# Optimization experiments

Hardware: AMD Instinct MI355X
Metric: run time of the kernel (lower is better)

The kernel has to match this reference:

```python
import jax, jax.numpy as jnp
import numpy as np

B, T, DK, DV = 64, 2048, 128, 128
INIT_SCALE = 0.01


def setup_inputs() -> dict:
    key = jax.random.key(0)
    ks = jax.random.split(key, 7)
    return {
        "query": jax.random.normal(ks[0], (B, T, DK), dtype=jnp.float32),
        "key": jax.random.normal(ks[1], (B, T, DK), dtype=jnp.float32),
        "value": jax.random.normal(ks[2], (B, T, DV), dtype=jnp.float32),
        "alpha": jax.random.uniform(ks[3], (B, T, 1), dtype=jnp.float32),
        "rho": jax.random.uniform(ks[4], (B, T, 1), dtype=jnp.float32),
        "lam": jax.random.uniform(ks[5], (B, T, 1), dtype=jnp.float32),
        "init_state": jax.random.normal(ks[6], (B, DK, DV), dtype=jnp.float32) * INIT_SCALE,
    }


def reference(query, key, value, alpha, rho, lam, init_state):
    """Decayed outer-product fast-weight memory, scanned over time.

    Per step t:  M_t = lam_t * M_{t-1} + (rho_t * alpha_t) * (k_t outer v_t)
                 r_t = q_t^T M_t                      # [B, D_v]
    Returns readouts [B, T, D_v].
    """
    # time-major inputs for scan: [T, B, ...]
    tm = lambda x: jnp.swapaxes(x, 0, 1)
    xs = (tm(query), tm(key), tm(value), tm(alpha), tm(rho), tm(lam))

    def step(M, inp):
        q, k, v, a, r, l = inp  # q,k: [B,DK]; v: [B,DV]; a,r,l: [B,1]
        write_scale = (r * a)[:, :, None]          # [B,1,1]
        outer = k[:, :, None] * v[:, None, :]      # [B,DK,DV]
        M = l[:, :, None] * M + write_scale * outer
        read = jnp.einsum('bk,bkv->bv', q, M)      # [B,DV]
        return M, read

    _, reads = jax.lax.scan(step, init_state, xs)
    return jnp.swapaxes(reads, 0, 1)  # [B,T,DV]
```

## Files before the change

### kernel.cpp

```cpp
#include <hip/hip_runtime.h>
#include <hip/hip_bf16.h>


typedef float  f32x4  __attribute__((ext_vector_type(4)));
typedef short  bf16x8 __attribute__((ext_vector_type(8)));
typedef short  bf16x4 __attribute__((ext_vector_type(4)));

constexpr int B_ = 64, T_ = 2048;
constexpr int NSPLIT = 8;
constexpr int CT = 64;
constexpr int NCH = T_ / CT;

__device__ __forceinline__ bf16x8 cvt8(float4 a, float4 b) {
  union { __hip_bfloat162 h2[4]; bf16x8 v; } u;
  u.h2[0] = __float22bfloat162_rn(make_float2(a.x, a.y));
  u.h2[1] = __float22bfloat162_rn(make_float2(a.z, a.w));
  u.h2[2] = __float22bfloat162_rn(make_float2(b.x, b.y));
  u.h2[3] = __float22bfloat162_rn(make_float2(b.z, b.w));
  return u.v;
}

__device__ __forceinline__ float fexp2(float x) { return __builtin_exp2f(x); }
__device__ __forceinline__ float flog2(float x) { return __builtin_log2f(x); }

#define MFMA(a, b, c) __builtin_amdgcn_mfma_f32_16x16x32_bf16((a), (b), (c), 0, 0, 0)

__global__ __launch_bounds__(256, 2) void lmm_2b(
    const float* __restrict__ q_g, const float* __restrict__ k_g,
    const float* __restrict__ v_g, const float* __restrict__ a_g,
    const float* __restrict__ r_g, const float* __restrict__ l_g,
    const float* __restrict__ m0_g, float* __restrict__ out_g)
{
  const int bid   = blockIdx.y * NSPLIT + blockIdx.x;
  const int b     = (bid & 7) * 8 + (bid >> 6);
  const int split = (bid >> 3) & 7;

  const int tid   = threadIdx.x;
  const int w     = tid >> 6;
  const int lane  = tid & 63;
  const int m     = lane & 15;
  const int quad  = lane >> 4;
  const int jbase = split * 16;

  __shared__ __align__(16) __hip_bfloat16 klds[2][64][136];
  __shared__ __align__(16) __hip_bfloat16 MhT [16][136];
  __shared__ __align__(16) __hip_bfloat16 VwT [16][72];
  __shared__ __align__(16) __hip_bfloat16 VwTd[16][72];
  __shared__ __align__(16) __hip_bfloat16 Sd[4][16][72];

  const float* qb = q_g + (size_t)b * T_ * 128;
  const float* kb = k_g + (size_t)b * T_ * 128;
  const float* vb = v_g + (size_t)b * T_ * 128;
  const float* ab = a_g + (size_t)b * T_;
  const float* rb = r_g + (size_t)b * T_;
  const float* lb = l_g + (size_t)b * T_;
  float*       ob = out_g + (size_t)b * T_ * 128;

  f32x4 M[2];
  #pragma unroll
  for (int it = 0; it < 2; ++it)
    #pragma unroll
    for (int r = 0; r < 4; ++r)
      M[it][r] = m0_g[((size_t)b * 128 + w * 32 + it * 16 + quad * 4 + r) * 128 +
                      jbase + m];

  const int jv   = tid & 15;
  const int s16  = tid >> 4;
  const int krow = tid >> 2;
  const int kc4  = tid & 3;

  float4 qpre[4][2];
  float4 kpre[8];
  float  vpre[4];
  float  lpre, apre, rpre;

  lpre = lb[lane]; apre = ab[lane]; rpre = rb[lane];
  #pragma unroll
  for (int f = 0; f < 8; ++f)
    kpre[f] = *(const float4*)&kb[(size_t)krow * 128 + kc4 * 32 + f * 4];
  #pragma unroll
  for (int ks = 0; ks < 4; ++ks) {
    const float* p = qb + (size_t)(w * 16 + m) * 128 + ks * 32 + quad * 8;
    qpre[ks][0] = *(const float4*)p;
    qpre[ks][1] = *(const float4*)(p + 4);
  }
  #pragma unroll
  for (int rep = 0; rep < 4; ++rep)
    vpre[rep] = vb[(size_t)(s16 * 4 + rep) * 128 + jbase + jv];
  #pragma unroll
  for (int g = 0; g < 4; ++g)
    *(bf16x8*)&klds[0][krow][kc4 * 32 + g * 8] =
        cvt8(kpre[2 * g], kpre[2 * g + 1]);

  #pragma unroll 2
  for (int ch = 0; ch < NCH; ++ch) {
    const int t0   = ch * CT;
    const int tn   = (ch + 1 < NCH) ? t0 + CT : t0;
    const int buf  = ch & 1;
    const int nbuf = buf ^ 1;

    __syncthreads();

    float x = flog2(fmaxf(lpre, 1e-20f));
    #pragma unroll
    for (int d = 1; d < 64; d <<= 1) {
      const float o = __shfl_up(x, d, 64);
      if (lane >= d) x += o;
    }
    const float L2    = x;
    const float L2end = __shfl(L2, 63, 64);
    const float arp   = apre * rpre;

    bf16x8 qf[4];
    #pragma unroll
    for (int ks = 0; ks < 4; ++ks) qf[ks] = cvt8(qpre[ks][0], qpre[ks][1]);

    const int tl0 = w * 16 + quad * 4;
    float tl[4];
    #pragma unroll
    for (int r = 0; r < 4; ++r) tl[r] = __shfl(L2, tl0 + r, 64);

    f32x4 S[4] = {{0.f,0.f,0.f,0.f},{0.f,0.f,0.f,0.f},
                  {0.f,0.f,0.f,0.f},{0.f,0.f,0.f,0.f}};
    #pragma unroll
    for (int sb = 0; sb < 4; ++sb) {
      const int rowk = sb * 16 + m;
      #pragma unroll
      for (int ks = 0; ks < 4; ++ks) {
        const bf16x8 kf = *(const bf16x8*)&klds[buf][rowk][ks * 32 + quad * 8];
        S[sb] = MFMA(qf[ks], kf, S[sb]);
      }
    }

    #pragma unroll
    for (int sb = 0; sb < 4; ++sb) {
      const int   sl_i = sb * 16 + m;
      const float sl   = __shfl(L2, sl_i, 64);
      #pragma unroll
      for (int r = 0; r < 4; ++r) {
        const float dv = (sl_i <= tl0 + r) ? S[sb][r] * fexp2(tl[r] - sl) : 0.f;
        Sd[w][quad * 4 + r][sl_i] = __float2bfloat16(dv);
      }
    }

    {
      float fw[4], fd[4];
      #pragma unroll
      for (int rep = 0; rep < 4; ++rep) {
        const int   s   = s16 * 4 + rep;
        const float arf = __shfl(arp, s, 64);
        const float dcf = fexp2(L2end - __shfl(L2, s, 64));
        fw[rep] = vpre[rep] * arf;
        fd[rep] = fw[rep] * dcf;
      }
      union { __hip_bfloat162 h2[2]; bf16x4 v; } uw, ud;
      uw.h2[0] = __float22bfloat162_rn(make_float2(fw[0], fw[1]));
      uw.h2[1] = __float22bfloat162_rn(make_float2(fw[2], fw[3]));
      ud.h2[0] = __float22bfloat162_rn(make_float2(fd[0], fd[1]));
      ud.h2[1] = __float22bfloat162_rn(make_float2(fd[2], fd[3]));
      *(bf16x4*)&VwT [jv][s16 * 4] = uw.v;
      *(bf16x4*)&VwTd[jv][s16 * 4] = ud.v;
    }

    #pragma unroll
    for (int it = 0; it < 2; ++it) {
      union { __hip_bfloat162 h2[2]; uint2 u; } pk;
      pk.h2[0] = __float22bfloat162_rn(make_float2(M[it][0], M[it][1]));
      pk.h2[1] = __float22bfloat162_rn(make_float2(M[it][2], M[it][3]));
      *(uint2*)&MhT[m][w * 32 + it * 16 + quad * 4] = pk.u;
    }

    __syncthreads();

    lpre = lb[tn + lane]; apre = ab[tn + lane]; rpre = rb[tn + lane];
    #pragma unroll
    for (int f = 0; f < 8; ++f)
      kpre[f] = *(const float4*)&kb[(size_t)(tn + krow) * 128 + kc4 * 32 + f * 4];
    #pragma unroll
    for (int ks = 0; ks < 4; ++ks) {
      const float* p = qb + (size_t)(tn + w * 16 + m) * 128 + ks * 32 + quad * 8;
      qpre[ks][0] = *(const float4*)p;
      qpre[ks][1] = *(const float4*)(p + 4);
    }
    #pragma unroll
    for (int rep = 0; rep < 4; ++rep)
      vpre[rep] = vb[(size_t)(tn + s16 * 4 + rep) * 128 + jbase + jv];

    f32x4 R = {0.f, 0.f, 0.f, 0.f};
    #pragma unroll
    for (int ks = 0; ks < 4; ++ks) {
      const bf16x8 mb = *(const bf16x8*)&MhT[m][ks * 32 + quad * 8];
      R = MFMA(qf[ks], mb, R);
    }
    #pragma unroll
    for (int r = 0; r < 4; ++r) R[r] *= fexp2(tl[r]);

    #pragma unroll
    for (int kk = 0; kk < 2; ++kk) {
      const bf16x8 sa = *(const bf16x8*)&Sd[w][m][kk * 32 + quad * 8];
      const bf16x8 vw = *(const bf16x8*)&VwT[m][kk * 32 + quad * 8];
      R = MFMA(sa, vw, R);
    }
    #pragma unroll
    for (int r = 0; r < 4; ++r)
      ob[(size_t)(t0 + w * 16 + quad * 4 + r) * 128 + jbase + m] = R[r];

    const float eend = fexp2(L2end);
    #pragma unroll
    for (int it = 0; it < 2; ++it)
      #pragma unroll
      for (int r = 0; r < 4; ++r) M[it][r] *= eend;
    #pragma unroll
    for (int kk = 0; kk < 2; ++kk) {
      const bf16x8 vd = *(const bf16x8*)&VwTd[m][kk * 32 + quad * 8];
      #pragma unroll
      for (int it = 0; it < 2; ++it) {
        union { __hip_bfloat16 h[8]; bf16x8 v; } ua;
        #pragma unroll
        for (int u = 0; u < 8; ++u)
          ua.h[u] = klds[buf][kk * 32 + quad * 8 + u][w * 32 + it * 16 + m];
        M[it] = MFMA(ua.v, vd, M[it]);
      }
    }

    #pragma unroll
    for (int g = 0; g < 4; ++g)
      *(bf16x8*)&klds[nbuf][krow][kc4 * 32 + g * 8] =
          cvt8(kpre[2 * g], kpre[2 * g + 1]);
  }
}

extern "C" void kernel_launch(void* const* d_in, const int* in_sizes, int n_in,
                              void* d_out, int out_size, void* d_ws, size_t ws_size,
                              hipStream_t stream) {
  const float* q  = (const float*)d_in[0];
  const float* k  = (const float*)d_in[1];
  const float* v  = (const float*)d_in[2];
  const float* a  = (const float*)d_in[3];
  const float* r  = (const float*)d_in[4];
  const float* l  = (const float*)d_in[5];
  const float* m0 = (const float*)d_in[6];
  float* out = (float*)d_out;

  dim3 grid(NSPLIT, B_);
  lmm_2b<<<grid, 256, 0, stream>>>(q, k, v, a, r, l, m0, out);
}
```

Before: 337.4 us.

## Stream K chunks via global_load_lds into swizzled fp32 LDS with explicit transpose

Loads of K chunks go directly from global memory into a single XOR-swizzled fp32 LDS buffer using global_load_lds, which removes the register-staged prefetch and bf16 conversion on store. Each chunk builds an explicit transposed bf16 copy (kT) for the state-update MFMA, in place of the old strided per-element gather. The log-decay prefix scan for the next chunk now runs at the end of the previous iteration, off the critical path, and the Sd writes are swizzled to reduce bank conflicts. In exchange the S-matrix MFMA converts fp32 K to bf16 on every read, the LDS footprint grows, and the loop is no longer unrolled.

```diff
diff --git a/kernel.cpp b/kernel.cpp
--- a/kernel.cpp
+++ b/kernel.cpp
@@ -25,7 +25,13 @@
 
 #define MFMA(a, b, c) __builtin_amdgcn_mfma_f32_16x16x32_bf16((a), (b), (c), 0, 0, 0)
 
-__global__ __launch_bounds__(256, 2) void lmm_2b(
+__device__ __forceinline__ void gload16(const float* gsrc, float* ldst) {
+  __builtin_amdgcn_global_load_lds(
+      (const __attribute__((address_space(1))) void*)gsrc,
+      (__attribute__((address_space(3))) void*)ldst, 16, 0, 0);
+}
+
+__global__ __launch_bounds__(256, 2) void lmm_v8(
     const float* __restrict__ q_g, const float* __restrict__ k_g,
     const float* __restrict__ v_g, const float* __restrict__ a_g,
     const float* __restrict__ r_g, const float* __restrict__ l_g,
@@ -42,8 +48,9 @@
   const int quad  = lane >> 4;
   const int jbase = split * 16;
 
-  __shared__ __align__(16) __hip_bfloat16 klds[2][64][136];
-  __shared__ __align__(16) __hip_bfloat16 MhT [16][136];
+  __shared__ __align__(16) float klds[64][128];
+  __shared__ __align__(16) __hip_bfloat16 kT [128][72];
+  __shared__ __align__(16) __hip_bfloat16 MhT[16][136];
   __shared__ __align__(16) __hip_bfloat16 VwT [16][72];
   __shared__ __align__(16) __hip_bfloat16 VwTd[16][72];
   __shared__ __align__(16) __hip_bfloat16 Sd[4][16][72];
@@ -66,18 +73,24 @@
 
   const int jv   = tid & 15;
   const int s16  = tid >> 4;
-  const int krow = tid >> 2;
-  const int kc4  = tid & 3;
+  const int prow = lane >> 5;
+  const int pblk = lane & 31;
+  const int ti   = lane + ((w & 1) << 6);
+  const int tsh  = w >> 1;
+  const int tl0  = w * 16 + quad * 4;
 
   float4 qpre[4][2];
-  float4 kpre[8];
   float  vpre[4];
   float  lpre, apre, rpre;
+  float  L2c, L2ec, tlc[4], arpc;
 
   lpre = lb[lane]; apre = ab[lane]; rpre = rb[lane];
   #pragma unroll
-  for (int f = 0; f < 8; ++f)
-    kpre[f] = *(const float4*)&kb[(size_t)krow * 128 + kc4 * 32 + f * 4];
+  for (int c = 0; c < 8; ++c) {
+    const int row = w * 16 + c * 2 + prow;
+    gload16(kb + (size_t)row * 128 + ((pblk ^ (row & 7)) << 2),
+            &klds[w * 16 + c * 2][0]);
+  }
   #pragma unroll
   for (int ks = 0; ks < 4; ++ks) {
     const float* p = qb + (size_t)(w * 16 + m) * 128 + ks * 32 + quad * 8;
@@ -87,59 +100,69 @@
   #pragma unroll
   for (int rep = 0; rep < 4; ++rep)
     vpre[rep] = vb[(size_t)(s16 * 4 + rep) * 128 + jbase + jv];
-  #pragma unroll
-  for (int g = 0; g < 4; ++g)
-    *(bf16x8*)&klds[0][krow][kc4 * 32 + g * 8] =
-        cvt8(kpre[2 * g], kpre[2 * g + 1]);
-
-  #pragma unroll 2
-  for (int ch = 0; ch < NCH; ++ch) {
-    const int t0   = ch * CT;
-    const int tn   = (ch + 1 < NCH) ? t0 + CT : t0;
-    const int buf  = ch & 1;
-    const int nbuf = buf ^ 1;
-
-    __syncthreads();
-
+  {
     float x = flog2(fmaxf(lpre, 1e-20f));
     #pragma unroll
     for (int d = 1; d < 64; d <<= 1) {
       const float o = __shfl_up(x, d, 64);
       if (lane >= d) x += o;
     }
-    const float L2    = x;
-    const float L2end = __shfl(L2, 63, 64);
-    const float arp   = apre * rpre;
+    L2c = x; L2ec = __shfl(L2c, 63, 64);
+    #pragma unroll
+    for (int r = 0; r < 4; ++r) tlc[r] = __shfl(L2c, tl0 + r, 64);
+    arpc = apre * rpre;
+  }
+
+  #pragma unroll 1
+  for (int ch = 0; ch < NCH; ++ch) {
+    const int t0 = ch * CT;
+    const int tn = (ch + 1 < NCH) ? t0 + CT : t0;
+
+    __syncthreads();
+
+    lpre = lb[tn + lane]; apre = ab[tn + lane]; rpre = rb[tn + lane];
+
+    #pragma unroll
+    for (int g = 0; g < 4; ++g) {
+      float kc[8];
+      #pragma unroll
+      for (int u2 = 0; u2 < 8; ++u2) {
+        const int row = tsh * 32 + g * 8 + u2;
+        kc[u2] = klds[row][((((ti >> 2) ^ (row & 7)) << 2) | (ti & 3))];
+      }
+      *(bf16x8*)&kT[ti][tsh * 32 + g * 8] =
+          cvt8(make_float4(kc[0], kc[1], kc[2], kc[3]),
+               make_float4(kc[4], kc[5], kc[6], kc[7]));
+    }
 
     bf16x8 qf[4];
     #pragma unroll
     for (int ks = 0; ks < 4; ++ks) qf[ks] = cvt8(qpre[ks][0], qpre[ks][1]);
-
-    const int tl0 = w * 16 + quad * 4;
-    float tl[4];
-    #pragma unroll
-    for (int r = 0; r < 4; ++r) tl[r] = __shfl(L2, tl0 + r, 64);
 
     f32x4 S[4] = {{0.f,0.f,0.f,0.f},{0.f,0.f,0.f,0.f},
                   {0.f,0.f,0.f,0.f},{0.f,0.f,0.f,0.f}};
     #pragma unroll
     for (int sb = 0; sb < 4; ++sb) {
       const int rowk = sb * 16 + m;
+      const int xk   = rowk & 7;
       #pragma unroll
       for (int ks = 0; ks < 4; ++ks) {
-        const bf16x8 kf = *(const bf16x8*)&klds[buf][rowk][ks * 32 + quad * 8];
-        S[sb] = MFMA(qf[ks], kf, S[sb]);
+        const int bk0 = ks * 8 + quad * 2;
+        const float4 kA = *(const float4*)&klds[rowk][((bk0      ^ xk) << 2)];
+        const float4 kB = *(const float4*)&klds[rowk][(((bk0 + 1) ^ xk) << 2)];
+        S[sb] = MFMA(qf[ks], cvt8(kA, kB), S[sb]);
       }
     }
 
     #pragma unroll
     for (int sb = 0; sb < 4; ++sb) {
       const int   sl_i = sb * 16 + m;
-      const float sl   = __shfl(L2, sl_i, 64);
+      const float sl   = __shfl(L2c, sl_i, 64);
       #pragma unroll
       for (int r = 0; r < 4; ++r) {
-        const float dv = (sl_i <= tl0 + r) ? S[sb][r] * fexp2(tl[r] - sl) : 0.f;
-        Sd[w][quad * 4 + r][sl_i] = __float2bfloat16(dv);
+        const float dv = (sl_i <= tl0 + r) ? S[sb][r] * fexp2(tlc[r] - sl) : 0.f;
+        Sd[w][quad * 4 + r][((((sl_i >> 3) ^ quad) << 3) | (sl_i & 7))] =
+            __float2bfloat16(dv);
       }
     }
 
@@ -148,8 +171,8 @@
       #pragma unroll
       for (int rep = 0; rep < 4; ++rep) {
         const int   s   = s16 * 4 + rep;
-        const float arf = __shfl(arp, s, 64);
-        const float dcf = fexp2(L2end - __shfl(L2, s, 64));
+        const float arf = __shfl(arpc, s, 64);
+        const float dcf = fexp2(L2ec - __shfl(L2c, s, 64));
         fw[rep] = vpre[rep] * arf;
         fd[rep] = fw[rep] * dcf;
       }
@@ -172,10 +195,12 @@
 
     __syncthreads();
 
-    lpre = lb[tn + lane]; apre = ab[tn + lane]; rpre = rb[tn + lane];
-    #pragma unroll
-    for (int f = 0; f < 8; ++f)
-      kpre[f] = *(const float4*)&kb[(size_t)(tn + krow) * 128 + kc4 * 32 + f * 4];
+    #pragma unroll
+    for (int c = 0; c < 8; ++c) {
+      const int row = w * 16 + c * 2 + prow;
+      gload16(kb + (size_t)(tn + row) * 128 + ((pblk ^ (row & 7)) << 2),
+              &klds[w * 16 + c * 2][0]);
+    }
     #pragma unroll
     for (int ks = 0; ks < 4; ++ks) {
       const float* p = qb + (size_t)(tn + w * 16 + m) * 128 + ks * 32 + quad * 8;
@@ -193,11 +218,12 @@
       R = MFMA(qf[ks], mb, R);
     }
     #pragma unroll
-    for (int r = 0; r < 4; ++r) R[r] *= fexp2(tl[r]);
+    for (int r = 0; r < 4; ++r) R[r] *= fexp2(tlc[r]);
 
     #pragma unroll
     for (int kk = 0; kk < 2; ++kk) {
-      const bf16x8 sa = *(const bf16x8*)&Sd[w][m][kk * 32 + quad * 8];
+      const bf16x8 sa = *(const bf16x8*)
+          &Sd[w][m][(((kk * 4 + quad) ^ ((m >> 2) & 3)) << 3)];
       const bf16x8 vw = *(const bf16x8*)&VwT[m][kk * 32 + quad * 8];
       R = MFMA(sa, vw, R);
     }
@@ -205,7 +231,7 @@
     for (int r = 0; r < 4; ++r)
       ob[(size_t)(t0 + w * 16 + quad * 4 + r) * 128 + jbase + m] = R[r];
 
-    const float eend = fexp2(L2end);
+    const float eend = fexp2(L2ec);
     #pragma unroll
     for (int it = 0; it < 2; ++it)
       #pragma unroll
@@ -215,18 +241,24 @@
       const bf16x8 vd = *(const bf16x8*)&VwTd[m][kk * 32 + quad * 8];
       #pragma unroll
       for (int it = 0; it < 2; ++it) {
-        union { __hip_bfloat16 h[8]; bf16x8 v; } ua;
-        #pragma unroll
-        for (int u = 0; u < 8; ++u)
-          ua.h[u] = klds[buf][kk * 32 + quad * 8 + u][w * 32 + it * 16 + m];
-        M[it] = MFMA(ua.v, vd, M[it]);
-      }
-    }
-
-    #pragma unroll
-    for (int g = 0; g < 4; ++g)
-      *(bf16x8*)&klds[nbuf][krow][kc4 * 32 + g * 8] =
-          cvt8(kpre[2 * g], kpre[2 * g + 1]);
+        const bf16x8 af =
+            *(const bf16x8*)&kT[w * 32 + it * 16 + m][kk * 32 + quad * 8];
+        M[it] = MFMA(af, vd, M[it]);
+      }
+    }
+
+    {
+      float x = flog2(fmaxf(lpre, 1e-20f));
+      #pragma unroll
+      for (int d = 1; d < 64; d <<= 1) {
+        const float o = __shfl_up(x, d, 64);
+        if (lane >= d) x += o;
+      }
+      L2c = x; L2ec = __shfl(L2c, 63, 64);
+      #pragma unroll
+      for (int r = 0; r < 4; ++r) tlc[r] = __shfl(L2c, tl0 + r, 64);
+      arpc = apre * rpre;
+    }
   }
 }
 
@@ -243,5 +275,5 @@
   float* out = (float*)d_out;
 
   dim3 grid(NSPLIT, B_);
-  lmm_2b<<<grid, 256, 0, stream>>>(q, k, v, a, r, l, m0, out);
-}
+  lmm_v8<<<grid, 256, 0, stream>>>(q, k, v, a, r, l, m0, out);
+}
```

Measured after the change: 324.0 us. -4.0%, faster.
